# Performance work log

Measured on AMD Instinct MI355X. Metric: run time of the kernel, lower is better.

## Reference

```python
import jax, jax.numpy as jnp
import numpy as np

L = 3          # atom_decoder_depth
HEADS = 8      # spatial attention heads
T_HEADS = 8    # temporal attention heads
WQ = 32        # atoms_per_window_queries
HK = 128       # atoms_per_window_keys
EPS = 1e-5


def _ln(x, g=None, b=None):
    mu = jnp.mean(x, -1, keepdims=True)
    v = jnp.mean((x - mu) ** 2, -1, keepdims=True)
    xn = (x - mu) * jax.lax.rsqrt(v + EPS)
    if g is not None:
        xn = xn * g + b
    return xn


def _adaln(a, s, w_sc, b_sc, w_sk):
    # adaptive LN: sigmoid-scaled normed activations + conditioned skip
    sn = _ln(s)
    return jax.nn.sigmoid(sn @ w_sc + b_sc) * _ln(a) + sn @ w_sk


def setup_inputs() -> dict:
    key = jax.random.key(0)
    ks = iter(jax.random.split(key, 64))
    B0, T, N, M, D, TS = 1, 8, 1024, 4096, 256, 768
    HID = 2 * D

    def rn(shape, s=1.0):
        return jax.random.normal(next(ks), shape, jnp.float32) * s

    NW = (M + WQ - 1) // WQ
    a = rn((B0 * T, N, 2 * TS))
    q = rn((B0 * T, M, D))
    c = rn((B0 * T, M, D))
    atom_dec_bias = rn((B0, NW, WQ, HK, L * HEADS), 0.1)
    tok_idx = jnp.sort(jax.random.randint(next(ks), (B0, M), 0, N), axis=-1)
    atom_to_token = jax.nn.one_hot(tok_idx, N, dtype=jnp.float32)
    atom_pad_mask = jnp.ones((B0, M), bool)
    timestamps = jnp.sort(jax.random.uniform(next(ks), (B0, T)) * 10.0, axis=-1)
    p = 0.02
    return dict(
        a=a, q=q, c=c, atom_dec_bias=atom_dec_bias,
        atom_to_token=atom_to_token, atom_pad_mask=atom_pad_mask,
        timestamps=timestamps,
        W_a2q=rn((2 * TS, D), p),
        ada1_sw=rn((L, D, D), p), ada1_sb=rn((L, D), p), ada1_kw=rn((L, D, D), p),
        attn_wq=rn((L, D, D), p), attn_bq=rn((L, D), p),
        attn_wk=rn((L, D, D), p), attn_wv=rn((L, D, D), p),
        attn_wg=rn((L, D, D), p), attn_wo=rn((L, D, D), p),
        og_w=rn((L, D, D), p), og_b=rn((L, D), p),
        ada2_sw=rn((L, D, D), p), ada2_sb=rn((L, D), p), ada2_kw=rn((L, D, D), p),
        tr_w1=rn((L, D, HID), p), tr_w2=rn((L, D, HID), p), tr_w3=rn((L, HID, D), p),
        tr_gw=rn((L, D, D), p), tr_gb=rn((L, D), p),
        t_ln_g=jnp.ones((L, D)), t_ln_b=jnp.zeros((L, D)),
        t_wq=rn((L, D, D), p), t_wk=rn((L, D, D), p), t_wv=rn((L, D, D), p),
        t_wg=rn((L, D, D), p), t_wo=rn((L, D, D), p),
        t_decay=rn((L, T_HEADS)),
        pos_g=jnp.ones((D,)), pos_b=jnp.zeros((D,)), pos_w=rn((D, 3), p),
        T=8,
    )


def _forward(a, q, c, atom_dec_bias, atom_to_token, atom_pad_mask, timestamps,
             W_a2q, ada1_sw, ada1_sb, ada1_kw, attn_wq, attn_bq, attn_wk,
             attn_wv, attn_wg, attn_wo, og_w, og_b, ada2_sw, ada2_sb, ada2_kw,
             tr_w1, tr_w2, tr_w3, tr_gw, tr_gb, t_ln_g, t_ln_b, t_wq, t_wk,
             t_wv, t_wg, t_wo, t_decay, pos_g, pos_b, pos_w, T):
    BT, N, _ = a.shape
    B0 = BT // T
    M0, D = q.shape[1], q.shape[2]
    NW = (M0 + WQ - 1) // WQ
    M = NW * WQ
    h, dh = HEADS, D // HEADS
    th, tdh = T_HEADS, D // T_HEADS

    # token -> atom gather via one-hot matmul (atom_to_token shared across T)
    a2q = jnp.einsum('bmn,btnd->btmd', atom_to_token,
                     (a @ W_a2q).reshape(B0, T, N, D)).reshape(BT, M0, D)
    q = q + a2q

    pad = M - M0
    qf = jnp.pad(q, ((0, 0), (0, pad), (0, 0)))
    cf = jnp.pad(c, ((0, 0), (0, pad), (0, 0)))
    mask = jnp.pad(atom_pad_mask, ((0, 0), (0, pad)))  # (B0, M)

    side = (HK - WQ) // 2
    # index map: query window w attends keys [w*WQ - side, w*WQ - side + HK)
    widx = jnp.arange(NW)[:, None] * WQ + jnp.arange(HK)[None, :]

    def window_keys(x):  # (B, M, D) -> (B, NW, HK, D)
        xp = jnp.pad(x, ((0, 0), (side, side), (0, 0)))
        return xp[:, widx]

    kmask = jnp.pad(mask, ((0, 0), (side, side)))[:, widx]  # (B0, NW, HK)
    neg = jnp.where(kmask[:, None, :, None, None, :], 0.0, -1e9)

    bias = atom_dec_bias.reshape(B0, NW, WQ, HK, L, HEADS)
    inv_s = 1.0 / np.sqrt(dh).astype(np.float32)
    inv_t = 1.0 / np.sqrt(tdh).astype(np.float32)
    dt = jnp.abs(timestamps[:, :, None] - timestamps[:, None, :])  # (B0,T,T)

    for i in range(L):
        # ---- spatial windowed attention with pair bias ----
        b = _adaln(qf, cf, ada1_sw[i], ada1_sb[i], ada1_kw[i])
        qh = (b @ attn_wq[i] + attn_bq[i]).reshape(BT, NW, WQ, h, dh)
        kin = window_keys(b)                                   # (BT,NW,HK,D)
        kh = (kin @ attn_wk[i]).reshape(BT, NW, HK, h, dh)
        vh = (kin @ attn_wv[i]).reshape(BT, NW, HK, h, dh)
        logits = jnp.einsum('bnqhd,bnkhd->bnhqk', qh, kh) * inv_s
        logits = logits.reshape(B0, T, NW, h, WQ, HK)
        logits = logits + bias[:, :, :, :, i].transpose(0, 1, 4, 2, 3)[:, None] + neg
        p_attn = jax.nn.softmax(logits, axis=-1).reshape(BT, NW, h, WQ, HK)
        o = jnp.einsum('bnhqk,bnkhd->bnqhd', p_attn, vh)
        g = jax.nn.sigmoid(b @ attn_wg[i]).reshape(BT, NW, WQ, h, dh)
        o = (g * o).reshape(BT, M, D) @ attn_wo[i]
        qf = qf + jax.nn.sigmoid(cf @ og_w[i] + og_b[i]) * o
        # conditioned SwiGLU transition
        t = _adaln(qf, cf, ada2_sw[i], ada2_sb[i], ada2_kw[i])
        x = jax.nn.silu(t @ tr_w1[i]) * (t @ tr_w2[i])
        qf = qf + jax.nn.sigmoid(cf @ tr_gw[i] + tr_gb[i]) * (x @ tr_w3[i])
        # ---- temporal attention with per-head decay bias ----
        xt = qf.reshape(B0, T, M, D).transpose(0, 2, 1, 3)     # (B0,M,T,D)
        xn = _ln(xt, t_ln_g[i], t_ln_b[i])
        tq = (xn @ t_wq[i]).reshape(B0, M, T, th, tdh)
        tk = (xn @ t_wk[i]).reshape(B0, M, T, th, tdh)
        tv = (xn @ t_wv[i]).reshape(B0, M, T, th, tdh)
        tl = jnp.einsum('bmqhd,bmkhd->bmhqk', tq, tk) * inv_t
        decay = jax.nn.softplus(t_decay[i])                    # (th,)
        tl = tl - decay[None, None, :, None, None] * dt[:, None, None]
        tp = jax.nn.softmax(tl, axis=-1)
        to = jnp.einsum('bmhqk,bmkhd->bmqhd', tp, tv).reshape(B0, M, T, D)
        tg = jax.nn.sigmoid(xn @ t_wg[i])
        xt = xt + (tg * to) @ t_wo[i]
        qf = xt.transpose(0, 2, 1, 3).reshape(BT, M, D)

    q_out = qf[:, :M0]
    return _ln(q_out, pos_g, pos_b) @ pos_w  # (B*T, M0, 3)


def reference(a, q, c, atom_dec_bias, atom_to_token, atom_pad_mask, timestamps,
              W_a2q, ada1_sw, ada1_sb, ada1_kw, attn_wq, attn_bq, attn_wk,
              attn_wv, attn_wg, attn_wo, og_w, og_b, ada2_sw, ada2_sb, ada2_kw,
              tr_w1, tr_w2, tr_w3, tr_gw, tr_gb, t_ln_g, t_ln_b, t_wq, t_wk,
              t_wv, t_wg, t_wo, t_decay, pos_g, pos_b, pos_w, T):
    return _forward(a, q, c, atom_dec_bias, atom_to_token, atom_pad_mask,
                    timestamps, W_a2q, ada1_sw, ada1_sb, ada1_kw, attn_wq,
                    attn_bq, attn_wk, attn_wv, attn_wg, attn_wo, og_w, og_b,
                    ada2_sw, ada2_sb, ada2_kw, tr_w1, tr_w2, tr_w3, tr_gw,
                    tr_gb, t_ln_g, t_ln_b, t_wq, t_wk, t_wv, t_wg, t_wo,
                    t_decay, pos_g, pos_b, pos_w, T)
```

## Files before the change

kernel.cpp:

```cpp
#include <hip/hip_runtime.h>
#include <cstddef>
#include <cstdint>

#define DEVI __device__ __forceinline__

typedef __attribute__((ext_vector_type(8))) __bf16 bf16x8;
typedef __attribute__((ext_vector_type(8))) unsigned short us8;
typedef __attribute__((ext_vector_type(4))) unsigned short us4;
typedef __attribute__((ext_vector_type(4))) float f32x4;

constexpr int B0_ = 1, T_ = 8, N_ = 1024, M_ = 4096, D_ = 256;
constexpr int BT_ = 8, NW_ = 128, WQ_ = 32, HK_ = 128, SIDE_ = 48;
constexpr int R_ = BT_ * M_;
constexpr size_t Fq = 8388608;

DEVI unsigned short f2b(float f) {
  return __builtin_bit_cast(unsigned short, static_cast<__bf16>(f));
}
DEVI float b2f(unsigned short s) { return __uint_as_float(((unsigned)s) << 16); }
DEVI float sigm(float x) { return 1.0f / (1.0f + __expf(-x)); }
DEVI bf16x8 ld_bf8(const unsigned short* p) {
  return __builtin_bit_cast(bf16x8, *(const us8*)p);
}
DEVI bf16x8 pack_f8(float4 v0, float4 v1) {
  bf16x8 r;
  r[0] = (__bf16)v0.x; r[1] = (__bf16)v0.y; r[2] = (__bf16)v0.z; r[3] = (__bf16)v0.w;
  r[4] = (__bf16)v1.x; r[5] = (__bf16)v1.y; r[6] = (__bf16)v1.z; r[7] = (__bf16)v1.w;
  return r;
}
DEVI void mfma_bf16(f32x4& c, bf16x8 a, bf16x8 b) {
  c = __builtin_amdgcn_mfma_f32_16x16x32_bf16(a, b, c, 0, 0, 0);
}
DEVI void gload16(const void* g, void* l) {
  __builtin_amdgcn_global_load_lds((__attribute__((address_space(1))) void*)g,
                                   (__attribute__((address_space(3))) void*)l, 16, 0, 0);
}

struct ConvArgs {
  const float* src[64];
  int doff[64];
  int Kd[64];
  int Nd[64];
  int n;
};

__global__ __launch_bounds__(256) void conv_k(ConvArgs ca, unsigned short* __restrict__ wbf) {
  int e = blockIdx.x;
  int K = ca.Kd[e], N = ca.Nd[e];
  int nx = N >> 6, nk = K >> 6;
  int t = blockIdx.y;
  if (t >= nx * nk) return;
  int tx = t % nx, tk = t / nx;
  const float* s = ca.src[e];
  unsigned short* d = wbf + ca.doff[e];
  int n = tx * 64 + (threadIdx.x & 63);
  int k0 = tk * 64 + (threadIdx.x >> 6) * 16;
  for (int r = 0; r < 16; r++) {
    int k = k0 + r;
    d[(size_t)n * K + k] = f2b(s[(size_t)k * N + n]);
  }
}

__global__ __launch_bounds__(256) void cvt_k(const float* __restrict__ s,
                                             unsigned short* __restrict__ d, int n8) {
  int i = blockIdx.x * 256 + threadIdx.x;
  if (i >= n8) return;
  float4 v0 = *(const float4*)(s + (size_t)i * 8);
  float4 v1 = *(const float4*)(s + (size_t)i * 8 + 4);
  *(us8*)(d + (size_t)i * 8) = __builtin_bit_cast(us8, pack_f8(v0, v1));
}

__global__ __launch_bounds__(256) void bias_prep_k(
    const float* __restrict__ bq, const float* __restrict__ sb1,
    const float* __restrict__ sb2, const float* __restrict__ ogb,
    const float* __restrict__ trb, float* __restrict__ bias) {
  int t = threadIdx.x;
  for (int i = t; i < 1024 + 3 * 2560; i += 256) bias[i] = 0.f;
  __syncthreads();
  for (int i = 0; i < 3; i++) {
    float* B = bias + 1024 + i * 2560;
    B[t]        = bq[i * 256 + t];
    B[1024 + t] = sb1[i * 256 + t];
    B[1536 + t] = sb2[i * 256 + t];
    B[2048 + t] = ogb[i * 256 + t];
    B[2304 + t] = trb[i * 256 + t];
  }
}

__global__ __launch_bounds__(256) void biasb_k(const float* __restrict__ adb,
                                               unsigned short* __restrict__ biasb) {
  __shared__ float ld[3072];
  int rq = blockIdx.x;
  int t = threadIdx.x;
  const float* src = adb + (size_t)rq * 3072;
  for (int i = t; i < 3072; i += 256) ld[i] = src[i];
  __syncthreads();
  int k = t & 127;
  for (int lh = t >> 7; lh < 24; lh += 2)
    biasb[((size_t)lh * 4096 + rq) * 128 + k] = f2b(ld[k * 24 + lh]);
}

__global__ __launch_bounds__(256) void tokidx_k(const float* __restrict__ a2t,
                                                int* __restrict__ idx) {
  int m = blockIdx.x * 4 + (threadIdx.x >> 6);
  int lane = threadIdx.x & 63;
  int best = -1;
  for (int j = 0; j < 16; j++) {
    int col = lane * 16 + j;
    if (a2t[(size_t)m * 1024 + col] > 0.5f) best = col;
  }
#pragma unroll
  for (int off = 1; off < 64; off <<= 1) best = max(best, __shfl_xor(best, off));
  if (lane == 0) idx[m] = best;
}

__global__ __launch_bounds__(256) void qfinitln_k(const float* __restrict__ q,
                                                  const unsigned short* __restrict__ tokf,
                                                  const int* __restrict__ idx,
                                                  float* __restrict__ qf,
                                                  unsigned short* __restrict__ lnout) {
  int wid = threadIdx.x >> 6, lane = threadIdx.x & 63;
  size_t row = (size_t)blockIdx.x * 4 + wid;
  int m = (int)(row & 4095);
  int bt = (int)(row >> 12);
  float4 qv = *(const float4*)(q + row * 256 + lane * 4);
  us4 tv = *(const us4*)(tokf + ((size_t)bt * 1024 + idx[m]) * 256 + lane * 4);
  float x[4];
  x[0] = qv.x + b2f(tv[0]); x[1] = qv.y + b2f(tv[1]);
  x[2] = qv.z + b2f(tv[2]); x[3] = qv.w + b2f(tv[3]);
  *(float4*)(qf + row * 256 + lane * 4) = make_float4(x[0], x[1], x[2], x[3]);
  float s = x[0] + x[1] + x[2] + x[3];
  float sq = x[0] * x[0] + x[1] * x[1] + x[2] * x[2] + x[3] * x[3];
#pragma unroll
  for (int o = 1; o < 64; o <<= 1) {
    s += __shfl_xor(s, o);
    sq += __shfl_xor(sq, o);
  }
  float mu = s * 0.00390625f;
  float rs = rsqrtf(sq * 0.00390625f - mu * mu + 1e-5f);
  us4 r;
#pragma unroll
  for (int j = 0; j < 4; j++) r[j] = f2b((x[j] - mu) * rs);
  *(us4*)(lnout + row * 256 + lane * 4) = r;
}

__global__ __launch_bounds__(256) void ln_k(const float* __restrict__ src,
                                            unsigned short* __restrict__ dst) {
  size_t row = (size_t)blockIdx.x * 4 + (threadIdx.x >> 6);
  int lane = threadIdx.x & 63;
  float4 v = ((const float4*)(src + row * 256))[lane];
  float s = v.x + v.y + v.z + v.w;
#pragma unroll
  for (int o = 1; o < 64; o <<= 1) s += __shfl_xor(s, o);
  float mu = s * 0.00390625f;
  float dx = v.x - mu, dy = v.y - mu, dz = v.z - mu, dw = v.w - mu;
  float qv = dx * dx + dy * dy + dz * dz + dw * dw;
#pragma unroll
  for (int o = 1; o < 64; o <<= 1) qv += __shfl_xor(qv, o);
  float rs = rsqrtf(qv * 0.00390625f + 1e-5f);
  us4 r;
  r[0] = f2b(dx * rs); r[1] = f2b(dy * rs); r[2] = f2b(dz * rs); r[3] = f2b(dw * rs);
  *(us4*)(dst + row * 256 + lane * 4) = r;
}

template <int K, int EP, int NI>
__global__ __launch_bounds__(256) void gemm3_k(
    const unsigned short* __restrict__ A, const unsigned short* __restrict__ Wt,
    const float* __restrict__ bias, unsigned short* __restrict__ out,
    const unsigned short* __restrict__ lnq, int NOUT) {
  constexpr bool DUAL = (EP == 4 || EP == 5);
  constexpr int PAIR = (EP == 4) ? 256 : 512;
  constexpr int BN = NI * 32;
  constexpr int BSZ = BN * 64;
  __shared__ __align__(16) unsigned short S[128 * 64 + BSZ + (DUAL ? BSZ : 0)];
  unsigned short* As = S;
  unsigned short* Bs = S + 128 * 64;
  unsigned short* Bs2 = Bs + BSZ;
  const int tid = threadIdx.x;
  const int lane = tid & 63, w = tid >> 6;
  const int lg = lane >> 4, lr = lane & 15;
  const int wr = w >> 1, wc = w & 1;
  const size_t m_base = (size_t)blockIdx.x * 128;
  const size_t n_base = (size_t)blockIdx.y * BN;
  const int srow = w * 8 + (lane >> 3);
  const int scol = ((lane & 7) ^ (lane >> 3)) * 8;
  const unsigned short* gA = A + (m_base + srow) * K + scol;
  const unsigned short* gB = Wt + (n_base + srow) * K + scol;
  const unsigned short* gB2 = Wt + (n_base + PAIR + srow) * K + scol;
  f32x4 acc[4][NI] = {};
  f32x4 acc2[DUAL ? 4 : 1][DUAL ? NI : 1] = {};
  const int swz = lr & 7;
  for (int kk = 0; kk < K; kk += 64) {
#pragma unroll
    for (int j = 0; j < 4; j++)
      gload16(gA + (size_t)(j * 32) * K + kk, As + w * 512 + j * 2048);
#pragma unroll
    for (int j = 0; j < NI; j++)
      gload16(gB + (size_t)(j * 32) * K + kk, Bs + w * 512 + j * 2048);
    if constexpr (DUAL) {
#pragma unroll
      for (int j = 0; j < NI; j++)
        gload16(gB2 + (size_t)(j * 32) * K + kk, Bs2 + w * 512 + j * 2048);
    }
    __syncthreads();
#pragma unroll
    for (int ks = 0; ks < 2; ks++) {
      const int co = ((ks * 4 + lg) ^ swz) << 3;
      bf16x8 af[4], b1[NI], b2v[NI];
#pragma unroll
      for (int i = 0; i < 4; i++) af[i] = ld_bf8(As + (wr * 64 + i * 16 + lr) * 64 + co);
#pragma unroll
      for (int i = 0; i < NI; i++) {
        b1[i] = ld_bf8(Bs + (wc * (BN / 2) + i * 16 + lr) * 64 + co);
        if constexpr (DUAL) b2v[i] = ld_bf8(Bs2 + (wc * (BN / 2) + i * 16 + lr) * 64 + co);
      }
#pragma unroll
      for (int mi = 0; mi < 4; mi++)
#pragma unroll
        for (int ni = 0; ni < NI; ni++) {
          mfma_bf16(acc[mi][ni], af[mi], b1[ni]);
          if constexpr (DUAL) mfma_bf16(acc2[mi][ni], af[mi], b2v[ni]);
        }
    }
    __syncthreads();
  }
#pragma unroll
  for (int mi = 0; mi < 4; mi++)
#pragma unroll
    for (int ni = 0; ni < NI; ni++)
#pragma unroll
      for (int r = 0; r < 4; r++) {
        int rowl = wr * 64 + mi * 16 + lg * 4 + r;
        int col = wc * (BN / 2) + ni * 16 + lr;
        size_t grow = m_base + rowl;
        int gcol = (int)n_base + col;
        float v = acc[mi][ni][r] + bias[gcol];
        unsigned short res;
        if constexpr (EP == 1) {
          res = f2b(v);
        } else if constexpr (EP == 4) {
          float vk = acc2[mi][ni][r] + bias[gcol + 256];
          res = f2b(sigm(v) * b2f(lnq[grow * 256 + gcol]) + vk);
        } else {
          float v2 = acc2[mi][ni][r] + bias[gcol + 512];
          res = f2b(v * sigm(v) * v2);
        }
        S[rowl * BN + (((col >> 3) ^ (rowl & 7)) << 3) + (col & 7)] = res;
      }
  __syncthreads();
  constexpr int CH = BN / 8;
#pragma unroll
  for (int p = 0; p < BN / 16; p++) {
    int rowl = p * (256 / CH) + tid / CH;
    int chunk = tid % CH;
    us8 v = *(const us8*)(S + rowl * BN + ((chunk ^ (rowl & 7)) << 3));
    *(us8*)(out + (m_base + rowl) * NOUT + n_base + chunk * 8) = v;
  }
}

template <int K, bool GATED>
__global__ __launch_bounds__(512) void gemmln_k(
    const unsigned short* __restrict__ A, const unsigned short* __restrict__ Wt,
    float* __restrict__ qf, const unsigned short* __restrict__ gate,
    unsigned short* __restrict__ lnout, const float* __restrict__ lng,
    const float* __restrict__ lnb) {
  __shared__ __align__(16) unsigned short S[64 * 64 + 256 * 64];
  unsigned short* As = S;
  unsigned short* Bs = S + 64 * 64;
  const int tid = threadIdx.x;
  const int lane = tid & 63, w = tid >> 6;
  const int lg = lane >> 4, lr = lane & 15;
  const size_t m_base = (size_t)blockIdx.x * 64;
  const int srow = lane >> 3;
  const int scol = ((lane & 7) ^ srow) * 8;
  const unsigned short* gA = A + (m_base + w * 8 + srow) * K + scol;
  const unsigned short* gB = Wt + (w * 32 + srow) * K + scol;
  f32x4 acc[4][2] = {};
  const int swz = lr & 7;
  for (int kk = 0; kk < K; kk += 64) {
    gload16(gA + kk, As + w * 512);
#pragma unroll
    for (int j = 0; j < 4; j++)
      gload16(gB + (size_t)(j * 8) * K + kk, Bs + w * 2048 + j * 512);
    __syncthreads();
#pragma unroll
    for (int ks = 0; ks < 2; ks++) {
      const int co = ((ks * 4 + lg) ^ swz) << 3;
      bf16x8 af[4], bf1[2];
#pragma unroll
      for (int i = 0; i < 4; i++) af[i] = ld_bf8(As + (i * 16 + lr) * 64 + co);
#pragma unroll
      for (int i = 0; i < 2; i++) bf1[i] = ld_bf8(Bs + (w * 32 + i * 16 + lr) * 64 + co);
#pragma unroll
      for (int mi = 0; mi < 4; mi++)
#pragma unroll
        for (int ni = 0; ni < 2; ni++) mfma_bf16(acc[mi][ni], af[mi], bf1[ni]);
    }
    __syncthreads();
  }
#pragma unroll
  for (int mi = 0; mi < 4; mi++)
#pragma unroll
    for (int ni = 0; ni < 2; ni++)
#pragma unroll
      for (int r = 0; r < 4; r++) {
        int rowl = mi * 16 + lg * 4 + r;
        int col = w * 32 + ni * 16 + lr;
        size_t grow = m_base + rowl;
        float v = acc[mi][ni][r];
        if constexpr (GATED) v *= sigm(b2f(gate[grow * 256 + col]));
        float nq = qf[grow * 256 + col] + v;
        qf[grow * 256 + col] = nq;
        S[rowl * 256 + (((col >> 3) ^ (rowl & 7)) << 3) + (col & 7)] = f2b(nq);
      }
  __syncthreads();
  float gv[4], bv[4];
  if (lng) {
#pragma unroll
    for (int j = 0; j < 4; j++) {
      gv[j] = lng[lane * 4 + j];
      bv[j] = lnb[lane * 4 + j];
    }
  }
  const int rchunk = ((lane >> 1)) ;
  const int rsub = (lane & 1) << 2;
  for (int rr = 0; rr < 8; rr++) {
    int rowl = w * 8 + rr;
    us4 vv = *(const us4*)(S + rowl * 256 + ((rchunk ^ (rowl & 7)) << 3) + rsub);
    float x[4];
#pragma unroll
    for (int j = 0; j < 4; j++) x[j] = b2f(vv[j]);
    float s = x[0] + x[1] + x[2] + x[3];
    float sq = x[0] * x[0] + x[1] * x[1] + x[2] * x[2] + x[3] * x[3];
#pragma unroll
    for (int o = 1; o < 64; o <<= 1) {
      s += __shfl_xor(s, o);
      sq += __shfl_xor(sq, o);
    }
    float mu = s * 0.00390625f;
    float rs = rsqrtf(sq * 0.00390625f - mu * mu + 1e-5f);
    us4 r;
#pragma unroll
    for (int j = 0; j < 4; j++) {
      float y = (x[j] - mu) * rs;
      if (lng) y = y * gv[j] + bv[j];
      r[j] = f2b(y);
    }
    *(us4*)(lnout + (m_base + rowl) * 256 + lane * 4) = r;
  }
}

__global__ __launch_bounds__(256) void attn_k(const unsigned short* __restrict__ big1,
                                              const unsigned short* __restrict__ biasb,
                                              unsigned short* __restrict__ o, int layer) {
  __shared__ __align__(16) unsigned short pl_s[4][32 * 128];
  __shared__ __align__(16) unsigned short vt_s[4][32 * 128];
  const int w = blockIdx.x, bt = blockIdx.y, hg = blockIdx.z;
  const int tid = threadIdx.x, wid = tid >> 6, lane = tid & 63;
  const int lg = lane >> 4, lr = lane & 15;
  const int h = hg * 4 + wid;
  unsigned short* pl = pl_s[wid];
  unsigned short* vt = vt_s[wid];
  const size_t base = (size_t)bt * M_;
  const float inv_s = 0.17677669529663687f;

  {
    const int chunk = lane & 3;
    const int krow = lane >> 2;
#pragma unroll
    for (int it = 0; it < 8; it++) {
      int key = it * 16 + krow;
      int ak = w * 32 - SIDE_ + key;
      int akc = ak < 0 ? 0 : (ak > M_ - 1 ? M_ - 1 : ak);
      us8 v = *(const us8*)(big1 + (base + akc) * 1024 + 512 + h * 32 + chunk * 8);
#pragma unroll
      for (int e = 0; e < 8; e++) {
        int d = chunk * 8 + e;
        vt[d * 128 + (key ^ ((d & 7) << 3))] = v[e];
      }
    }
  }
  bf16x8 aq[2];
#pragma unroll
  for (int mi = 0; mi < 2; mi++)
    aq[mi] = ld_bf8(big1 + (base + w * 32 + mi * 16 + lr) * 1024 + h * 32 + lg * 8);
  f32x4 lac[2][8] = {};
#pragma unroll
  for (int ni = 0; ni < 8; ni++) {
    int kidx = ni * 16 + lr;
    int ak = w * 32 - SIDE_ + kidx;
    int akc = ak < 0 ? 0 : (ak > M_ - 1 ? M_ - 1 : ak);
    bf16x8 bk = ld_bf8(big1 + (base + akc) * 1024 + 256 + h * 32 + lg * 8);
    mfma_bf16(lac[0][ni], aq[0], bk);
    mfma_bf16(lac[1][ni], aq[1], bk);
  }
  const unsigned short* brow0 =
      biasb + (((size_t)(layer * 8 + h)) * 4096 + w * 32) * 128;
#pragma unroll
  for (int mi = 0; mi < 2; mi++)
#pragma unroll
    for (int r = 0; r < 4; r++) {
      int qrow = mi * 16 + lg * 4 + r;
      const unsigned short* brow = brow0 + (size_t)qrow * 128;
      float lv[8];
      float mx = -3e38f;
#pragma unroll
      for (int ni = 0; ni < 8; ni++) {
        int kidx = ni * 16 + lr;
        int ak = w * 32 - SIDE_ + kidx;
        float x = lac[mi][ni][r] * inv_s + b2f(brow[kidx]) +
                  ((unsigned)ak < (unsigned)M_ ? 0.f : -1e9f);
        lv[ni] = x;
        mx = fmaxf(mx, x);
      }
#pragma unroll
      for (int off = 1; off < 16; off <<= 1) mx = fmaxf(mx, __shfl_xor(mx, off));
      float sum = 0.f;
#pragma unroll
      for (int ni = 0; ni < 8; ni++) {
        float e = __expf(lv[ni] - mx);
        lv[ni] = e;
        sum += e;
      }
#pragma unroll
      for (int off = 1; off < 16; off <<= 1) sum += __shfl_xor(sum, off);
      float inv = 1.f / sum;
      int sw = (qrow & 7) << 3;
#pragma unroll
      for (int ni = 0; ni < 8; ni++)
        pl[qrow * 128 + ((ni * 16 + lr) ^ sw)] = f2b(lv[ni] * inv);
    }
  f32x4 oc[2][2] = {};
#pragma unroll
  for (int ks = 0; ks < 4; ks++) {
    int kbase = ks * 32 + lg * 8;
    int kswz = kbase ^ ((lr & 7) << 3);
    bf16x8 ap0 = ld_bf8(pl + lr * 128 + kswz);
    bf16x8 ap1 = ld_bf8(pl + (16 + lr) * 128 + kswz);
    bf16x8 bv0 = ld_bf8(vt + lr * 128 + kswz);
    bf16x8 bv1 = ld_bf8(vt + (16 + lr) * 128 + kswz);
    mfma_bf16(oc[0][0], ap0, bv0);
    mfma_bf16(oc[0][1], ap0, bv1);
    mfma_bf16(oc[1][0], ap1, bv0);
    mfma_bf16(oc[1][1], ap1, bv1);
  }
#pragma unroll
  for (int mi = 0; mi < 2; mi++)
#pragma unroll
    for (int nd = 0; nd < 2; nd++)
#pragma unroll
      for (int r = 0; r < 4; r++) {
        int qrow = mi * 16 + lg * 4 + r;
        int d = nd * 16 + lr;
        size_t rowi = base + w * 32 + qrow;
        float gv = sigm(b2f(big1[rowi * 1024 + 768 + h * 32 + d]));
        o[rowi * 256 + h * 32 + d] = f2b(oc[mi][nd][r] * gv);
      }
}

__global__ __launch_bounds__(256) void tattn_k(const unsigned short* __restrict__ big1,
                                               const float* __restrict__ ts,
                                               const float* __restrict__ tdec,
                                               unsigned short* __restrict__ o, int layer) {
  __shared__ __align__(16) unsigned short lds[4][8 * 768];
  int wid = threadIdx.x >> 6, lane = threadIdx.x & 63;
  int m = blockIdx.x * 4 + wid;
  unsigned short* Lp = lds[wid];
  for (int it = 0; it < 12; it++) {
    int u = it * 64 + lane;
    int t = u / 96, pos = (u % 96) * 8;
    *(uint4*)(Lp + t * 768 + pos) =
        *(const uint4*)(big1 + ((size_t)(t * M_ + m)) * 1024 + pos);
  }
  __syncthreads();
  int th = lane >> 3, qt = lane & 7;
  float decay = log1pf(__expf(tdec[layer * 8 + th]));
  float tsq = ts[qt];
  const float inv_t = 0.17677669529663687f;
  float tqv[32];
#pragma unroll
  for (int d = 0; d < 32; d++) tqv[d] = b2f(Lp[qt * 768 + th * 32 + d]);
  float lv[8];
  float mx = -3e38f;
#pragma unroll
  for (int kt = 0; kt < 8; kt++) {
    float dot = 0.f;
#pragma unroll
    for (int d = 0; d < 32; d++) dot += tqv[d] * b2f(Lp[kt * 768 + 256 + th * 32 + d]);
    float x = dot * inv_t - decay * fabsf(tsq - ts[kt]);
    lv[kt] = x;
    mx = fmaxf(mx, x);
  }
  float s = 0.f;
#pragma unroll
  for (int kt = 0; kt < 8; kt++) {
    float e = __expf(lv[kt] - mx);
    lv[kt] = e;
    s += e;
  }
  float inv = 1.f / s;
  float tov[32];
#pragma unroll
  for (int d = 0; d < 32; d++) tov[d] = 0.f;
#pragma unroll
  for (int kt = 0; kt < 8; kt++) {
    float p = lv[kt] * inv;
#pragma unroll
    for (int d = 0; d < 32; d++) tov[d] += p * b2f(Lp[kt * 768 + 512 + th * 32 + d]);
  }
  size_t orow = (size_t)qt * M_ + m;
#pragma unroll
  for (int d = 0; d < 32; d++) {
    float tg = sigm(b2f(big1[orow * 1024 + 768 + th * 32 + d]));
    o[orow * 256 + th * 32 + d] = f2b(tov[d] * tg);
  }
}

__global__ __launch_bounds__(256) void final_k(const float* __restrict__ qf,
                                               const float* __restrict__ pg,
                                               const float* __restrict__ pb,
                                               const float* __restrict__ pw,
                                               float* __restrict__ out) {
  size_t row = (size_t)blockIdx.x * 4 + (threadIdx.x >> 6);
  int lane = threadIdx.x & 63;
  float4 v = ((const float4*)(qf + row * 256))[lane];
  float s = v.x + v.y + v.z + v.w;
#pragma unroll
  for (int o = 1; o < 64; o <<= 1) s += __shfl_xor(s, o);
  float mu = s * 0.00390625f;
  float dx = v.x - mu, dy = v.y - mu, dz = v.z - mu, dw = v.w - mu;
  float qv = dx * dx + dy * dy + dz * dz + dw * dw;
#pragma unroll
  for (int o = 1; o < 64; o <<= 1) qv += __shfl_xor(qv, o);
  float rs = rsqrtf(qv * 0.00390625f + 1e-5f);
  int d = lane * 4;
  float xn[4];
  xn[0] = dx * rs * pg[d] + pb[d];
  xn[1] = dy * rs * pg[d + 1] + pb[d + 1];
  xn[2] = dz * rs * pg[d + 2] + pb[d + 2];
  xn[3] = dw * rs * pg[d + 3] + pb[d + 3];
  float p0 = 0.f, p1 = 0.f, p2 = 0.f;
#pragma unroll
  for (int dd = 0; dd < 4; dd++) {
    const float* wr = pw + (size_t)(d + dd) * 3;
    p0 += xn[dd] * wr[0];
    p1 += xn[dd] * wr[1];
    p2 += xn[dd] * wr[2];
  }
#pragma unroll
  for (int o = 1; o < 64; o <<= 1) {
    p0 += __shfl_xor(p0, o);
    p1 += __shfl_xor(p1, o);
    p2 += __shfl_xor(p2, o);
  }
  if (lane == 0) {
    out[row * 3 + 0] = p0;
    out[row * 3 + 1] = p1;
    out[row * 3 + 2] = p2;
  }
}

extern "C" void kernel_launch(void* const* d_in, const int* in_sizes, int n_in,
                              void* d_out, int out_size, void* d_ws, size_t ws_size,
                              hipStream_t stream) {
  const float* a       = (const float*)d_in[0];
  const float* q_in    = (const float*)d_in[1];
  const float* c_in    = (const float*)d_in[2];
  const float* adb     = (const float*)d_in[3];
  const float* a2t     = (const float*)d_in[4];
  const float* ts      = (const float*)d_in[6];
  const float* W_a2q   = (const float*)d_in[7];
  const float* ada1_sw = (const float*)d_in[8];
  const float* ada1_sb = (const float*)d_in[9];
  const float* ada1_kw = (const float*)d_in[10];
  const float* attn_wq = (const float*)d_in[11];
  const float* attn_bq = (const float*)d_in[12];
  const float* attn_wk = (const float*)d_in[13];
  const float* attn_wv = (const float*)d_in[14];
  const float* attn_wg = (const float*)d_in[15];
  const float* attn_wo = (const float*)d_in[16];
  const float* og_w    = (const float*)d_in[17];
  const float* og_b    = (const float*)d_in[18];
  const float* ada2_sw = (const float*)d_in[19];
  const float* ada2_sb = (const float*)d_in[20];
  const float* ada2_kw = (const float*)d_in[21];
  const float* tr_w1   = (const float*)d_in[22];
  const float* tr_w2   = (const float*)d_in[23];
  const float* tr_w3   = (const float*)d_in[24];
  const float* tr_gw   = (const float*)d_in[25];
  const float* tr_gb   = (const float*)d_in[26];
  const float* t_ln_g  = (const float*)d_in[27];
  const float* t_ln_b  = (const float*)d_in[28];
  const float* t_wq    = (const float*)d_in[29];
  const float* t_wk    = (const float*)d_in[30];
  const float* t_wv    = (const float*)d_in[31];
  const float* t_wg    = (const float*)d_in[32];
  const float* t_wo    = (const float*)d_in[33];
  const float* t_dec   = (const float*)d_in[34];
  const float* pos_g   = (const float*)d_in[35];
  const float* pos_b   = (const float*)d_in[36];
  const float* pos_w   = (const float*)d_in[37];

  char* base = (char*)d_ws;
  size_t off = 0;
  auto alloc = [&](size_t bytes) {
    void* p = base + off;
    off += (bytes + 255) & ~(size_t)255;
    return p;
  };
  float* qf            = (float*)alloc(Fq * 4);
  unsigned short* lncb = (unsigned short*)alloc(Fq * 2);
  unsigned short* lnqb = (unsigned short*)alloc(Fq * 2);
  unsigned short* obuf = (unsigned short*)alloc(Fq * 2);
  unsigned short* big1 = (unsigned short*)alloc(Fq * 8);
  unsigned short* bbuf = (unsigned short*)alloc(Fq * 2);
  unsigned short* ggate= (unsigned short*)alloc(Fq * 2);
  unsigned short* cbf  = (unsigned short*)alloc(Fq * 2);
  unsigned short* biasb= (unsigned short*)alloc((size_t)24 * 4096 * 128 * 2);
  unsigned short* wbf  = (unsigned short*)alloc((size_t)4718592 * 2);
  float* biasr         = (float*)alloc(8704 * 4);
  int* tokidx          = (int*)alloc(4096 * 4);

  unsigned short* xbuf = big1;
  unsigned short* abf  = big1;
  unsigned short* tokf = big1 + 2 * Fq;

  ConvArgs ca;
  int ne = 0;
  auto add = [&](const float* s, size_t doff, int K, int N) {
    ca.src[ne] = s; ca.doff[ne] = (int)doff; ca.Kd[ne] = K; ca.Nd[ne] = N; ne++;
  };
  constexpr size_t LW = 1441792;
  for (int i = 0; i < 3; i++) {
    size_t LB = (size_t)i * LW;
    add(ada1_sw + i * 65536, LB + 0, 256, 256);
    add(ada1_kw + i * 65536, LB + 65536, 256, 256);
    add(attn_wq + i * 65536, LB + 131072, 256, 256);
    add(attn_wk + i * 65536, LB + 196608, 256, 256);
    add(attn_wv + i * 65536, LB + 262144, 256, 256);
    add(attn_wg + i * 65536, LB + 327680, 256, 256);
    add(attn_wo + i * 65536, LB + 393216, 256, 256);
    add(og_w + i * 65536, LB + 458752, 256, 256);
    add(tr_gw + i * 65536, LB + 524288, 256, 256);
    add(ada2_sw + i * 65536, LB + 589824, 256, 256);
    add(ada2_kw + i * 65536, LB + 655360, 256, 256);
    add(tr_w1 + i * 131072, LB + 720896, 256, 512);
    add(tr_w2 + i * 131072, LB + 851968, 256, 512);
    add(tr_w3 + i * 131072, LB + 983040, 512, 256);
    add(t_wq + i * 65536, LB + 1114112, 256, 256);
    add(t_wk + i * 65536, LB + 1179648, 256, 256);
    add(t_wv + i * 65536, LB + 1245184, 256, 256);
    add(t_wg + i * 65536, LB + 1310720, 256, 256);
    add(t_wo + i * 65536, LB + 1376256, 256, 256);
  }
  add(W_a2q, 3 * LW, 1536, 256);
  ca.n = ne;

  conv_k<<<dim3(ne, 96), 256, 0, stream>>>(ca, wbf);
  bias_prep_k<<<1, 256, 0, stream>>>(attn_bq, ada1_sb, ada2_sb, og_b, tr_gb, biasr);
  tokidx_k<<<1024, 256, 0, stream>>>(a2t, tokidx);
  biasb_k<<<4096, 256, 0, stream>>>(adb, biasb);
  cvt_k<<<6144, 256, 0, stream>>>(a, abf, 1572864);
  cvt_k<<<4096, 256, 0, stream>>>(c_in, cbf, 1048576);
  gemm3_k<1536, 1, 2><<<dim3(64, 4), 256, 0, stream>>>(
      abf, wbf + 3 * LW, biasr, tokf, nullptr, 256);
  qfinitln_k<<<8192, 256, 0, stream>>>(q_in, tokf, tokidx, qf, lnqb);
  ln_k<<<8192, 256, 0, stream>>>(c_in, lncb);

  for (int i = 0; i < 3; i++) {
    size_t LB = (size_t)i * LW;
    const float* b_attn = biasr + 1024 + (size_t)i * 2560;
    const float* b_ada1 = b_attn + 1024;
    const float* b_ada2 = b_attn + 1536;
    const float* b_ogtr = b_attn + 2048;

    gemm3_k<256, 4, 4><<<dim3(256, 2), 256, 0, stream>>>(
        lncb, wbf + LB, b_ada1, bbuf, lnqb, 256);
    gemm3_k<256, 1, 4><<<dim3(256, 8), 256, 0, stream>>>(
        bbuf, wbf + LB + 131072, b_attn, big1, nullptr, 1024);
    attn_k<<<dim3(128, 8, 2), 256, 0, stream>>>(big1, biasb, obuf, i);
    gemm3_k<256, 1, 4><<<dim3(256, 2), 256, 0, stream>>>(
        cbf, wbf + LB + 458752, b_ogtr, ggate, nullptr, 256);
    gemmln_k<256, true><<<512, 512, 0, stream>>>(
        obuf, wbf + LB + 393216, qf, ggate, lnqb, nullptr, nullptr);
    gemm3_k<256, 4, 4><<<dim3(256, 2), 256, 0, stream>>>(
        lncb, wbf + LB + 589824, b_ada2, bbuf, lnqb, 256);
    gemm3_k<256, 5, 4><<<dim3(256, 4), 256, 0, stream>>>(
        bbuf, wbf + LB + 720896, biasr, xbuf, nullptr, 512);
    gemm3_k<256, 1, 4><<<dim3(256, 2), 256, 0, stream>>>(
        cbf, wbf + LB + 524288, b_ogtr + 256, ggate, nullptr, 256);
    gemmln_k<512, true><<<512, 512, 0, stream>>>(
        xbuf, wbf + LB + 983040, qf, ggate, lnqb,
        t_ln_g + (size_t)i * 256, t_ln_b + (size_t)i * 256);
    gemm3_k<256, 1, 4><<<dim3(256, 8), 256, 0, stream>>>(
        lnqb, wbf + LB + 1114112, biasr, big1, nullptr, 1024);
    tattn_k<<<1024, 256, 0, stream>>>(big1, ts, t_dec, obuf, i);
    gemmln_k<256, false><<<512, 512, 0, stream>>>(
        obuf, wbf + LB + 1376256, qf, nullptr, lnqb, nullptr, nullptr);
  }
  final_k<<<8192, 256, 0, stream>>>(qf, pos_g, pos_b, pos_w, (float*)d_out);
}
```

Before: 1.319 ms.

## Double-buffer GEMM LDS tiles and merge the two gate projections

Both GEMM kernels now use two LDS buffers, so the global load of the next K tile is issued while the current tile is being computed, replacing the single-buffer load/sync/compute loop. The generic GEMM becomes a dual-B kernel with a 64-column tile, and plain GEMMs compute two column halves per block. The og and transition gate projections, which use adjacent weights, are merged into one launch that writes a 512-wide gate buffer placed inside big1; the fused LN GEMMs read it through a column offset. The larger LDS footprint (64–80 KB per block) may reduce occupancy.

After: 1.153 ms. 1.14x faster.

```diff
diff --git a/kernel.cpp b/kernel.cpp
--- a/kernel.cpp
+++ b/kernel.cpp
@@ -163,110 +163,143 @@
   *(us4*)(dst + row * 256 + lane * 4) = r;
 }
 
-template <int K, int EP, int NI>
-__global__ __launch_bounds__(256) void gemm3_k(
+template <int K, int EP, int PAIR>
+__global__ __launch_bounds__(256) void gemm4_k(
     const unsigned short* __restrict__ A, const unsigned short* __restrict__ Wt,
     const float* __restrict__ bias, unsigned short* __restrict__ out,
     const unsigned short* __restrict__ lnq, int NOUT) {
-  constexpr bool DUAL = (EP == 4 || EP == 5);
-  constexpr int PAIR = (EP == 4) ? 256 : 512;
-  constexpr int BN = NI * 32;
-  constexpr int BSZ = BN * 64;
-  __shared__ __align__(16) unsigned short S[128 * 64 + BSZ + (DUAL ? BSZ : 0)];
-  unsigned short* As = S;
-  unsigned short* Bs = S + 128 * 64;
-  unsigned short* Bs2 = Bs + BSZ;
+  constexpr int NT = K / 64;
+  __shared__ __align__(16) unsigned short S[2][16384];
   const int tid = threadIdx.x;
   const int lane = tid & 63, w = tid >> 6;
   const int lg = lane >> 4, lr = lane & 15;
   const int wr = w >> 1, wc = w & 1;
   const size_t m_base = (size_t)blockIdx.x * 128;
-  const size_t n_base = (size_t)blockIdx.y * BN;
+  const size_t n_base = (size_t)blockIdx.y * 64;
   const int srow = w * 8 + (lane >> 3);
   const int scol = ((lane & 7) ^ (lane >> 3)) * 8;
   const unsigned short* gA = A + (m_base + srow) * K + scol;
   const unsigned short* gB = Wt + (n_base + srow) * K + scol;
   const unsigned short* gB2 = Wt + (n_base + PAIR + srow) * K + scol;
-  f32x4 acc[4][NI] = {};
-  f32x4 acc2[DUAL ? 4 : 1][DUAL ? NI : 1] = {};
+  f32x4 acc[4][2] = {};
+  f32x4 acc2[4][2] = {};
   const int swz = lr & 7;
-  for (int kk = 0; kk < K; kk += 64) {
+
+  auto stage = [&](int buf, int t) {
+    unsigned short* Sb = S[buf];
+    const int kk = t * 64;
 #pragma unroll
     for (int j = 0; j < 4; j++)
-      gload16(gA + (size_t)(j * 32) * K + kk, As + w * 512 + j * 2048);
-#pragma unroll
-    for (int j = 0; j < NI; j++)
-      gload16(gB + (size_t)(j * 32) * K + kk, Bs + w * 512 + j * 2048);
-    if constexpr (DUAL) {
-#pragma unroll
-      for (int j = 0; j < NI; j++)
-        gload16(gB2 + (size_t)(j * 32) * K + kk, Bs2 + w * 512 + j * 2048);
-    }
-    __syncthreads();
+      gload16(gA + (size_t)(j * 32) * K + kk, Sb + w * 512 + j * 2048);
+#pragma unroll
+    for (int j = 0; j < 2; j++)
+      gload16(gB + (size_t)(j * 32) * K + kk, Sb + 8192 + w * 512 + j * 2048);
+#pragma unroll
+    for (int j = 0; j < 2; j++)
+      gload16(gB2 + (size_t)(j * 32) * K + kk, Sb + 12288 + w * 512 + j * 2048);
+  };
+  auto compute = [&](int buf) {
+    const unsigned short* Sb = S[buf];
 #pragma unroll
     for (int ks = 0; ks < 2; ks++) {
       const int co = ((ks * 4 + lg) ^ swz) << 3;
-      bf16x8 af[4], b1[NI], b2v[NI];
-#pragma unroll
-      for (int i = 0; i < 4; i++) af[i] = ld_bf8(As + (wr * 64 + i * 16 + lr) * 64 + co);
-#pragma unroll
-      for (int i = 0; i < NI; i++) {
-        b1[i] = ld_bf8(Bs + (wc * (BN / 2) + i * 16 + lr) * 64 + co);
-        if constexpr (DUAL) b2v[i] = ld_bf8(Bs2 + (wc * (BN / 2) + i * 16 + lr) * 64 + co);
+      bf16x8 af[4], b1[2], b2[2];
+#pragma unroll
+      for (int i = 0; i < 4; i++)
+        af[i] = ld_bf8(Sb + (wr * 64 + i * 16 + lr) * 64 + co);
+#pragma unroll
+      for (int i = 0; i < 2; i++) {
+        b1[i] = ld_bf8(Sb + 8192 + (wc * 32 + i * 16 + lr) * 64 + co);
+        b2[i] = ld_bf8(Sb + 12288 + (wc * 32 + i * 16 + lr) * 64 + co);
       }
 #pragma unroll
       for (int mi = 0; mi < 4; mi++)
 #pragma unroll
-        for (int ni = 0; ni < NI; ni++) {
+        for (int ni = 0; ni < 2; ni++) {
           mfma_bf16(acc[mi][ni], af[mi], b1[ni]);
-          if constexpr (DUAL) mfma_bf16(acc2[mi][ni], af[mi], b2v[ni]);
+          mfma_bf16(acc2[mi][ni], af[mi], b2[ni]);
         }
     }
+  };
+
+  stage(0, 0);
+  __syncthreads();
+  int cur = 0;
+  for (int t = 0; t < NT - 1; t++) {
+    stage(cur ^ 1, t + 1);
+    compute(cur);
     __syncthreads();
-  }
-#pragma unroll
-  for (int mi = 0; mi < 4; mi++)
-#pragma unroll
-    for (int ni = 0; ni < NI; ni++)
-#pragma unroll
-      for (int r = 0; r < 4; r++) {
-        int rowl = wr * 64 + mi * 16 + lg * 4 + r;
-        int col = wc * (BN / 2) + ni * 16 + lr;
-        size_t grow = m_base + rowl;
-        int gcol = (int)n_base + col;
-        float v = acc[mi][ni][r] + bias[gcol];
-        unsigned short res;
-        if constexpr (EP == 1) {
-          res = f2b(v);
-        } else if constexpr (EP == 4) {
-          float vk = acc2[mi][ni][r] + bias[gcol + 256];
-          res = f2b(sigm(v) * b2f(lnq[grow * 256 + gcol]) + vk);
-        } else {
-          float v2 = acc2[mi][ni][r] + bias[gcol + 512];
-          res = f2b(v * sigm(v) * v2);
+    cur ^= 1;
+  }
+  compute(cur);
+  __syncthreads();
+
+  unsigned short* St = S[0];
+  if constexpr (EP == 1) {
+#pragma unroll
+    for (int half = 0; half < 2; half++) {
+      int cbase = (int)n_base + half * PAIR;
+#pragma unroll
+      for (int mi = 0; mi < 4; mi++)
+#pragma unroll
+        for (int ni = 0; ni < 2; ni++)
+#pragma unroll
+          for (int r = 0; r < 4; r++) {
+            int rowl = wr * 64 + mi * 16 + lg * 4 + r;
+            int cl = wc * 32 + ni * 16 + lr;
+            float v = (half ? acc2[mi][ni][r] : acc[mi][ni][r]) + bias[cbase + cl];
+            St[rowl * 64 + (((cl >> 3) ^ (rowl & 7)) << 3) + (cl & 7)] = f2b(v);
+          }
+      __syncthreads();
+#pragma unroll
+      for (int p = 0; p < 4; p++) {
+        int rowl = p * 32 + (tid >> 3);
+        int chunk = tid & 7;
+        us8 v = *(const us8*)(St + rowl * 64 + ((chunk ^ (rowl & 7)) << 3));
+        *(us8*)(out + (m_base + rowl) * NOUT + cbase + chunk * 8) = v;
+      }
+      __syncthreads();
+    }
+  } else {
+#pragma unroll
+    for (int mi = 0; mi < 4; mi++)
+#pragma unroll
+      for (int ni = 0; ni < 2; ni++)
+#pragma unroll
+        for (int r = 0; r < 4; r++) {
+          int rowl = wr * 64 + mi * 16 + lg * 4 + r;
+          int cl = wc * 32 + ni * 16 + lr;
+          size_t grow = m_base + rowl;
+          int gcol = (int)n_base + cl;
+          float v = acc[mi][ni][r] + bias[gcol];
+          float v2 = acc2[mi][ni][r] + bias[gcol + PAIR];
+          unsigned short res;
+          if constexpr (EP == 4) {
+            res = f2b(sigm(v) * b2f(lnq[grow * 256 + gcol]) + v2);
+          } else {
+            res = f2b(v * sigm(v) * v2);
+          }
+          St[rowl * 64 + (((cl >> 3) ^ (rowl & 7)) << 3) + (cl & 7)] = res;
         }
-        S[rowl * BN + (((col >> 3) ^ (rowl & 7)) << 3) + (col & 7)] = res;
-      }
-  __syncthreads();
-  constexpr int CH = BN / 8;
-#pragma unroll
-  for (int p = 0; p < BN / 16; p++) {
-    int rowl = p * (256 / CH) + tid / CH;
-    int chunk = tid % CH;
-    us8 v = *(const us8*)(S + rowl * BN + ((chunk ^ (rowl & 7)) << 3));
-    *(us8*)(out + (m_base + rowl) * NOUT + n_base + chunk * 8) = v;
+    __syncthreads();
+#pragma unroll
+    for (int p = 0; p < 4; p++) {
+      int rowl = p * 32 + (tid >> 3);
+      int chunk = tid & 7;
+      us8 v = *(const us8*)(St + rowl * 64 + ((chunk ^ (rowl & 7)) << 3));
+      *(us8*)(out + (m_base + rowl) * NOUT + n_base + chunk * 8) = v;
+    }
   }
 }
 
 template <int K, bool GATED>
 __global__ __launch_bounds__(512) void gemmln_k(
     const unsigned short* __restrict__ A, const unsigned short* __restrict__ Wt,
-    float* __restrict__ qf, const unsigned short* __restrict__ gate,
+    float* __restrict__ qf, const unsigned short* __restrict__ gate, int goff,
     unsigned short* __restrict__ lnout, const float* __restrict__ lng,
     const float* __restrict__ lnb) {
-  __shared__ __align__(16) unsigned short S[64 * 64 + 256 * 64];
-  unsigned short* As = S;
-  unsigned short* Bs = S + 64 * 64;
+  constexpr int NT = K / 64;
+  __shared__ __align__(16) unsigned short S[2][20480];
   const int tid = threadIdx.x;
   const int lane = tid & 63, w = tid >> 6;
   const int lg = lane >> 4, lr = lane & 15;
@@ -277,27 +310,46 @@
   const unsigned short* gB = Wt + (w * 32 + srow) * K + scol;
   f32x4 acc[4][2] = {};
   const int swz = lr & 7;
-  for (int kk = 0; kk < K; kk += 64) {
-    gload16(gA + kk, As + w * 512);
+
+  auto stage = [&](int buf, int t) {
+    unsigned short* Sb = S[buf];
+    const int kk = t * 64;
+    gload16(gA + kk, Sb + w * 512);
 #pragma unroll
     for (int j = 0; j < 4; j++)
-      gload16(gB + (size_t)(j * 8) * K + kk, Bs + w * 2048 + j * 512);
-    __syncthreads();
+      gload16(gB + (size_t)(j * 8) * K + kk, Sb + 4096 + w * 2048 + j * 512);
+  };
+  auto compute = [&](int buf) {
+    const unsigned short* Sb = S[buf];
 #pragma unroll
     for (int ks = 0; ks < 2; ks++) {
       const int co = ((ks * 4 + lg) ^ swz) << 3;
       bf16x8 af[4], bf1[2];
 #pragma unroll
-      for (int i = 0; i < 4; i++) af[i] = ld_bf8(As + (i * 16 + lr) * 64 + co);
-#pragma unroll
-      for (int i = 0; i < 2; i++) bf1[i] = ld_bf8(Bs + (w * 32 + i * 16 + lr) * 64 + co);
+      for (int i = 0; i < 4; i++) af[i] = ld_bf8(Sb + (i * 16 + lr) * 64 + co);
+#pragma unroll
+      for (int i = 0; i < 2; i++)
+        bf1[i] = ld_bf8(Sb + 4096 + (w * 32 + i * 16 + lr) * 64 + co);
 #pragma unroll
       for (int mi = 0; mi < 4; mi++)
 #pragma unroll
         for (int ni = 0; ni < 2; ni++) mfma_bf16(acc[mi][ni], af[mi], bf1[ni]);
     }
+  };
+
+  stage(0, 0);
+  __syncthreads();
+  int cur = 0;
+  for (int t = 0; t < NT - 1; t++) {
+    stage(cur ^ 1, t + 1);
+    compute(cur);
     __syncthreads();
-  }
+    cur ^= 1;
+  }
+  compute(cur);
+  __syncthreads();
+
+  unsigned short* St = S[0];
 #pragma unroll
   for (int mi = 0; mi < 4; mi++)
 #pragma unroll
@@ -308,10 +360,10 @@
         int col = w * 32 + ni * 16 + lr;
         size_t grow = m_base + rowl;
         float v = acc[mi][ni][r];
-        if constexpr (GATED) v *= sigm(b2f(gate[grow * 256 + col]));
+        if constexpr (GATED) v *= sigm(b2f(gate[grow * 512 + goff + col]));
         float nq = qf[grow * 256 + col] + v;
         qf[grow * 256 + col] = nq;
-        S[rowl * 256 + (((col >> 3) ^ (rowl & 7)) << 3) + (col & 7)] = f2b(nq);
+        St[rowl * 256 + (((col >> 3) ^ (rowl & 7)) << 3) + (col & 7)] = f2b(nq);
       }
   __syncthreads();
   float gv[4], bv[4];
@@ -322,11 +374,11 @@
       bv[j] = lnb[lane * 4 + j];
     }
   }
-  const int rchunk = ((lane >> 1)) ;
+  const int rchunk = lane >> 1;
   const int rsub = (lane & 1) << 2;
   for (int rr = 0; rr < 8; rr++) {
     int rowl = w * 8 + rr;
-    us4 vv = *(const us4*)(S + rowl * 256 + ((rchunk ^ (rowl & 7)) << 3) + rsub);
+    us4 vv = *(const us4*)(St + rowl * 256 + ((rchunk ^ (rowl & 7)) << 3) + rsub);
     float x[4];
 #pragma unroll
     for (int j = 0; j < 4; j++) x[j] = b2f(vv[j]);
@@ -614,16 +666,16 @@
   unsigned short* obuf = (unsigned short*)alloc(Fq * 2);
   unsigned short* big1 = (unsigned short*)alloc(Fq * 8);
   unsigned short* bbuf = (unsigned short*)alloc(Fq * 2);
-  unsigned short* ggate= (unsigned short*)alloc(Fq * 2);
   unsigned short* cbf  = (unsigned short*)alloc(Fq * 2);
   unsigned short* biasb= (unsigned short*)alloc((size_t)24 * 4096 * 128 * 2);
   unsigned short* wbf  = (unsigned short*)alloc((size_t)4718592 * 2);
   float* biasr         = (float*)alloc(8704 * 4);
   int* tokidx          = (int*)alloc(4096 * 4);
 
-  unsigned short* xbuf = big1;
-  unsigned short* abf  = big1;
-  unsigned short* tokf = big1 + 2 * Fq;
+  unsigned short* xbuf  = big1;
+  unsigned short* ggate = big1 + (size_t)R_ * 512;
+  unsigned short* abf   = big1;
+  unsigned short* tokf  = big1 + 2 * Fq;
 
   ConvArgs ca;
   int ne = 0;
@@ -662,7 +714,7 @@
   biasb_k<<<4096, 256, 0, stream>>>(adb, biasb);
   cvt_k<<<6144, 256, 0, stream>>>(a, abf, 1572864);
   cvt_k<<<4096, 256, 0, stream>>>(c_in, cbf, 1048576);
-  gemm3_k<1536, 1, 2><<<dim3(64, 4), 256, 0, stream>>>(
+  gemm4_k<1536, 1, 128><<<dim3(64, 2), 256, 0, stream>>>(
       abf, wbf + 3 * LW, biasr, tokf, nullptr, 256);
   qfinitln_k<<<8192, 256, 0, stream>>>(q_in, tokf, tokidx, qf, lnqb);
   ln_k<<<8192, 256, 0, stream>>>(c_in, lncb);
@@ -674,29 +726,27 @@
     const float* b_ada2 = b_attn + 1536;
     const float* b_ogtr = b_attn + 2048;
 
-    gemm3_k<256, 4, 4><<<dim3(256, 2), 256, 0, stream>>>(
+    gemm4_k<256, 4, 256><<<dim3(256, 4), 256, 0, stream>>>(
         lncb, wbf + LB, b_ada1, bbuf, lnqb, 256);
-    gemm3_k<256, 1, 4><<<dim3(256, 8), 256, 0, stream>>>(
+    gemm4_k<256, 1, 512><<<dim3(256, 8), 256, 0, stream>>>(
         bbuf, wbf + LB + 131072, b_attn, big1, nullptr, 1024);
     attn_k<<<dim3(128, 8, 2), 256, 0, stream>>>(big1, biasb, obuf, i);
-    gemm3_k<256, 1, 4><<<dim3(256, 2), 256, 0, stream>>>(
-        cbf, wbf + LB + 458752, b_ogtr, ggate, nullptr, 256);
+    gemm4_k<256, 1, 256><<<dim3(256, 4), 256, 0, stream>>>(
+        cbf, wbf + LB + 458752, b_ogtr, ggate, nullptr, 512);
     gemmln_k<256, true><<<512, 512, 0, stream>>>(
-        obuf, wbf + LB + 393216, qf, ggate, lnqb, nullptr, nullptr);
-    gemm3_k<256, 4, 4><<<dim3(256, 2), 256, 0, stream>>>(
+        obuf, wbf + LB + 393216, qf, ggate, 0, lnqb, nullptr, nullptr);
+    gemm4_k<256, 4, 256><<<dim3(256, 4), 256, 0, stream>>>(
         lncb, wbf + LB + 589824, b_ada2, bbuf, lnqb, 256);
-    gemm3_k<256, 5, 4><<<dim3(256, 4), 256, 0, stream>>>(
+    gemm4_k<256, 5, 512><<<dim3(256, 8), 256, 0, stream>>>(
         bbuf, wbf + LB + 720896, biasr, xbuf, nullptr, 512);
-    gemm3_k<256, 1, 4><<<dim3(256, 2), 256, 0, stream>>>(
-        cbf, wbf + LB + 524288, b_ogtr + 256, ggate, nullptr, 256);
     gemmln_k<512, true><<<512, 512, 0, stream>>>(
-        xbuf, wbf + LB + 983040, qf, ggate, lnqb,
+        xbuf, wbf + LB + 983040, qf, ggate, 256, lnqb,
         t_ln_g + (size_t)i * 256, t_ln_b + (size_t)i * 256);
-    gemm3_k<256, 1, 4><<<dim3(256, 8), 256, 0, stream>>>(
+    gemm4_k<256, 1, 512><<<dim3(256, 8), 256, 0, stream>>>(
         lnqb, wbf + LB + 1114112, biasr, big1, nullptr, 1024);
     tattn_k<<<1024, 256, 0, stream>>>(big1, ts, t_dec, obuf, i);
     gemmln_k<256, false><<<512, 512, 0, stream>>>(
-        obuf, wbf + LB + 1376256, qf, nullptr, lnqb, nullptr, nullptr);
+        obuf, wbf + LB + 1376256, qf, nullptr, 0, lnqb, nullptr, nullptr);
   }
   final_k<<<8192, 256, 0, stream>>>(qf, pos_g, pos_b, pos_w, (float*)d_out);
 }
```
